# Kernel tuning notes

Measured on AMD Instinct MI355X. Metric: run time of the kernel, lower is better.

Reference implementation:

```python
import jax, jax.numpy as jnp
import numpy as np

B, T, F, D = 2, 1, 2112, 1024
H, DH = 8, 64
INNER = H * DH
NL = 721           # cls_dim(1) + num_latents(720)
VD = 64            # vis_dim // 4
DEPTH = 6
MAX_FRAMES = 2160
EPS = 1e-5
W_SCALE = 0.02


def _ln(x, g, b):
    m = jnp.mean(x, axis=-1, keepdims=True)
    v = jnp.mean(jnp.square(x - m), axis=-1, keepdims=True)
    return (x - m) * jax.lax.rsqrt(v + EPS) * g + b


def setup_inputs() -> dict:
    key = jax.random.key(0)
    ks = jax.random.split(key, 12)
    n = lambda k, shape, s=1.0: jax.random.normal(k, shape, dtype=jnp.float32) * s
    inp = {}
    inp['x'] = n(ks[0], (B, T, F, D))
    inp['split_sizes'] = jax.random.randint(ks[1], (B,), 0, F, dtype=jnp.int32)
    # resampler parameters (randn init like torch)
    inp['latents'] = n(ks[2], (NL, D))
    inp['spatial_embs'] = n(ks[3], (VD + 1, D))
    inp['frame_embs'] = n(ks[4], (MAX_FRAMES, D))
    # per-layer attention params (stacked over depth)
    inp['nm_g'] = jnp.ones((DEPTH, D)); inp['nm_b'] = jnp.zeros((DEPTH, D))
    inp['nl_g'] = jnp.ones((DEPTH, D)); inp['nl_b'] = jnp.zeros((DEPTH, D))
    inp['wq'] = n(ks[5], (DEPTH, D, INNER), W_SCALE)
    inp['wkv'] = n(ks[6], (DEPTH, D, 2 * INNER), W_SCALE)
    inp['wo'] = n(ks[7], (DEPTH, INNER, D), W_SCALE)
    # per-layer FFN params
    inp['ffn_g'] = jnp.ones((DEPTH, D)); inp['ffn_b'] = jnp.zeros((DEPTH, D))
    inp['ffw1'] = n(ks[8], (DEPTH, D, 4 * D), W_SCALE)
    inp['ffw2'] = n(ks[9], (DEPTH, 4 * D, D), W_SCALE)
    # final norm
    inp['final_g'] = jnp.ones((D,)); inp['final_b'] = jnp.zeros((D,))
    return inp


def reference(x, split_sizes, latents, spatial_embs, frame_embs,
              nm_g, nm_b, nl_g, nl_b, wq, wkv, wo,
              ffn_g, ffn_b, ffw1, ffw2, final_g, final_b):
    b, t, f, d = x.shape
    # spatial embeddings: first VD tokens get rows [:VD], rest get row [VD] broadcast
    add_sp = jnp.concatenate(
        [spatial_embs[:VD], jnp.broadcast_to(spatial_embs[VD:VD + 1], (f - VD, d))], axis=0)
    # frame embeddings: first VD tokens get row 0, frames get rows 1..f-VD
    add_fr = jnp.concatenate(
        [jnp.broadcast_to(frame_embs[0:1], (VD, d)), frame_embs[1:f - VD + 1]], axis=0)
    x = x + (add_sp + add_fr)  # broadcast over (b, t)

    lat = jnp.broadcast_to(latents, (b, t, NL, d))

    # variable-length mask over the x part of KV; latent positions never masked
    mask_x = jnp.arange(f)[None, :] >= split_sizes[:, None]              # (b, f)
    mask = jnp.concatenate([mask_x, jnp.zeros((b, NL), dtype=bool)], -1)  # (b, f+NL)
    mask = mask[:, None, None, None, :]                                   # (b,1,1,1,j)
    scale = DH ** -0.5

    for l in range(DEPTH):
        # --- PerceiverAttention ---
        xn = _ln(x, nm_g[l], nm_b[l])
        latn = _ln(lat, nl_g[l], nl_b[l])
        q = (latn @ wq[l]).reshape(b, t, NL, H, DH) * scale
        kv = jnp.concatenate([xn, latn], axis=-2) @ wkv[l]               # (b,t,f+NL,2*inner)
        k, v = jnp.split(kv, 2, axis=-1)
        k = k.reshape(b, t, f + NL, H, DH)
        v = v.reshape(b, t, f + NL, H, DH)
        sim = jnp.einsum('btihd,btjhd->bhtij', q, k)                     # (b,h,t,NL,f+NL)
        sim = sim - jax.lax.stop_gradient(jnp.max(sim, axis=-1, keepdims=True))
        sim = jnp.where(mask, -jnp.inf, sim)
        attn = jax.nn.softmax(sim, axis=-1)
        o = jnp.einsum('bhtij,btjhd->btihd', attn, v).reshape(b, t, NL, INNER)
        lat = lat + o @ wo[l]
        # --- FeedForward ---
        h1 = _ln(lat, ffn_g[l], ffn_b[l]) @ ffw1[l]
        lat = lat + jax.nn.gelu(h1, approximate=False) @ ffw2[l]

    return _ln(lat, final_g, final_b)
```

## Files before the change

kernel.cpp:

```cpp
#include <hip/hip_runtime.h>
#include <math.h>

constexpr int B = 2;
constexpr int F = 2112;
constexpr int D = 1024;
constexpr int H = 8;
constexpr int DH = 64;
constexpr int INNER = H * DH;
constexpr int NL = 721;
constexpr int NL_PAD = 768;
constexpr int MLAT = B * NL;
constexpr int MLAT_PAD = 1536;
constexpr int VD = 64;
constexpr int DEPTH = 6;
constexpr int FN = F + NL;
constexpr int FN_PAD = 2880;
constexpr int NBH = B * H;
constexpr int SKVMAX = 8;
constexpr int MX = B * F;
constexpr float EPS = 1e-5f;

typedef __bf16 bf16x8 __attribute__((ext_vector_type(8)));
typedef float  f32x4  __attribute__((ext_vector_type(4)));

static __device__ __forceinline__ unsigned short f2bf(float f)
{
    union { float f; unsigned int u; } x; x.f = f;
    unsigned int r = x.u + 0x7FFFu + ((x.u >> 16) & 1u);
    return (unsigned short)(r >> 16);
}
static __device__ __forceinline__ float bf2f(unsigned short u)
{
    union { unsigned int i; float f; } x; x.i = ((unsigned int)u) << 16; return x.f;
}

static __device__ __forceinline__ int xcd_swz(int b, int nt)
{
    return (b & 7) * (nt >> 3) + (b >> 3);
}

__device__ __forceinline__ void block_reduce_2(float& s, float& ss, float* red)
{
#pragma unroll
    for (int off = 32; off; off >>= 1) {
        s  += __shfl_xor(s, off);
        ss += __shfl_xor(ss, off);
    }
    int wv = threadIdx.x >> 6;
    if ((threadIdx.x & 63) == 0) { red[wv] = s; red[4 + wv] = ss; }
    __syncthreads();
    s  = red[0] + red[1] + red[2] + red[3];
    ss = red[4] + red[5] + red[6] + red[7];
}

__global__ __launch_bounds__(256) void emb_ln_kernel(
    const float* __restrict__ x, const float* __restrict__ sp_emb,
    const float* __restrict__ fr_emb, unsigned short* __restrict__ xhat)
{
    __shared__ float red[8];
    int r = blockIdx.x;
    int j = r % F;
    int t = threadIdx.x;
    const float4* xr = (const float4*)(x + (long)r * D);
    int spr = (j < VD) ? j : VD;
    int frr = (j < VD) ? 0 : (j - VD + 1);
    const float4* sp4 = (const float4*)(sp_emb + (long)spr * D);
    const float4* fr4 = (const float4*)(fr_emb + (long)frr * D);
    float4 v = xr[t], a = sp4[t], c = fr4[t];
    v.x += a.x + c.x; v.y += a.y + c.y; v.z += a.z + c.z; v.w += a.w + c.w;
    float s  = v.x + v.y + v.z + v.w;
    float ss = v.x*v.x + v.y*v.y + v.z*v.z + v.w*v.w;
    block_reduce_2(s, ss, red);
    float mean = s * (1.0f / D);
    float var  = ss * (1.0f / D) - mean * mean;
    float rstd = rsqrtf(var + EPS);
    ushort4 o;
    o.x = f2bf((v.x - mean) * rstd);
    o.y = f2bf((v.y - mean) * rstd);
    o.z = f2bf((v.z - mean) * rstd);
    o.w = f2bf((v.w - mean) * rstd);
    ((ushort4*)(xhat + (long)r * D))[t] = o;
}

__global__ __launch_bounds__(256) void prep_a_kernel(
    const unsigned short* __restrict__ xhat, const float* __restrict__ lat,
    const float* __restrict__ nmg, const float* __restrict__ nmb,
    const float* __restrict__ nlg, const float* __restrict__ nlb,
    unsigned short* __restrict__ xa, unsigned short* __restrict__ la)
{
    __shared__ float red[8];
    int r = blockIdx.x;
    int t = threadIdx.x;
    if (r < MX) {
        ushort4 u4 = ((const ushort4*)(xhat + (long)r * D))[t];
        float4 g4 = ((const float4*)nmg)[t];
        float4 b4 = ((const float4*)nmb)[t];
        ushort4 o;
        o.x = f2bf(bf2f(u4.x) * g4.x + b4.x);
        o.y = f2bf(bf2f(u4.y) * g4.y + b4.y);
        o.z = f2bf(bf2f(u4.z) * g4.z + b4.z);
        o.w = f2bf(bf2f(u4.w) * g4.w + b4.w);
        ((ushort4*)(xa + (long)r * D))[t] = o;
    } else {
        int rr = r - MX;
        float4 v = ((const float4*)(lat + (long)rr * D))[t];
        float s  = v.x + v.y + v.z + v.w;
        float ss = v.x*v.x + v.y*v.y + v.z*v.z + v.w*v.w;
        block_reduce_2(s, ss, red);
        float mean = s * (1.0f / D);
        float var  = ss * (1.0f / D) - mean * mean;
        float rstd = rsqrtf(var + EPS);
        float4 g4 = ((const float4*)nlg)[t];
        float4 b4 = ((const float4*)nlb)[t];
        ushort4 o;
        o.x = f2bf((v.x - mean) * rstd * g4.x + b4.x);
        o.y = f2bf((v.y - mean) * rstd * g4.y + b4.y);
        o.z = f2bf((v.z - mean) * rstd * g4.z + b4.z);
        o.w = f2bf((v.w - mean) * rstd * g4.w + b4.w);
        ((ushort4*)(la + (long)rr * D))[t] = o;
    }
}

__global__ __launch_bounds__(256) void rownorm_affine_bf16_kernel(
    const float* __restrict__ in, const float* __restrict__ g,
    const float* __restrict__ b, unsigned short* __restrict__ out)
{
    __shared__ float red[8];
    int r = blockIdx.x;
    int t = threadIdx.x;
    float4 v = ((const float4*)(in + (long)r * D))[t];
    float s  = v.x + v.y + v.z + v.w;
    float ss = v.x*v.x + v.y*v.y + v.z*v.z + v.w*v.w;
    block_reduce_2(s, ss, red);
    float mean = s * (1.0f / D);
    float var  = ss * (1.0f / D) - mean * mean;
    float rstd = rsqrtf(var + EPS);
    float4 g4 = ((const float4*)g)[t];
    float4 b4 = ((const float4*)b)[t];
    ushort4 o;
    o.x = f2bf((v.x - mean) * rstd * g4.x + b4.x);
    o.y = f2bf((v.y - mean) * rstd * g4.y + b4.y);
    o.z = f2bf((v.z - mean) * rstd * g4.z + b4.z);
    o.w = f2bf((v.w - mean) * rstd * g4.w + b4.w);
    ((ushort4*)(out + (long)r * D))[t] = o;
}

__global__ __launch_bounds__(256) void final_ln_kernel(
    const float* __restrict__ in, const float* __restrict__ g,
    const float* __restrict__ b, float* __restrict__ out)
{
    __shared__ float red[8];
    int r = blockIdx.x;
    int t = threadIdx.x;
    float4 v = ((const float4*)(in + (long)r * D))[t];
    float s  = v.x + v.y + v.z + v.w;
    float ss = v.x*v.x + v.y*v.y + v.z*v.z + v.w*v.w;
    block_reduce_2(s, ss, red);
    float mean = s * (1.0f / D);
    float var  = ss * (1.0f / D) - mean * mean;
    float rstd = rsqrtf(var + EPS);
    float4 g4 = ((const float4*)g)[t];
    float4 b4 = ((const float4*)b)[t];
    float4 o;
    o.x = (v.x - mean) * rstd * g4.x + b4.x;
    o.y = (v.y - mean) * rstd * g4.y + b4.y;
    o.z = (v.z - mean) * rstd * g4.z + b4.z;
    o.w = (v.w - mean) * rstd * g4.w + b4.w;
    ((float4*)(out + (long)r * D))[t] = o;
}

__global__ __launch_bounds__(256) void lat_init_kernel(
    const float* __restrict__ latents, float* __restrict__ lat)
{
    int r = blockIdx.x;
    int i = r % NL;
    int t = threadIdx.x;
    ((float4*)(lat + (long)r * D))[t] = ((const float4*)(latents + (long)i * D))[t];
}

constexpr long WL_LAT = 1536L * 1024;
constexpr long WL_WO  = 1024L * 512;
constexpr long WL_F1  = 4096L * 1024;
constexpr long WL_F2  = 1024L * 4096;
constexpr long WL_SZ  = WL_LAT + WL_WO + WL_F1 + WL_F2;

__device__ __forceinline__ void conv_tile64(
    const float* __restrict__ src, unsigned short* __restrict__ dst,
    int Kd, int Nd, int tn, int tk, float* lds)
{
    int t = threadIdx.x;
    int n0 = tn * 64, k0 = tk * 64;
#pragma unroll
    for (int p = 0; p < 16; ++p) {
        int idx = p * 256 + t;
        int kr = idx >> 6, nc = idx & 63;
        lds[nc * 65 + kr] = src[(long)(k0 + kr) * Nd + n0 + nc];
    }
    __syncthreads();
#pragma unroll
    for (int p = 0; p < 2; ++p) {
        int nl_ = p * 32 + (t >> 3);
        int kc  = t & 7;
        unsigned short u[8];
#pragma unroll
        for (int j = 0; j < 8; ++j)
            u[j] = f2bf(lds[nl_ * 65 + kc * 8 + j]);
        *(uint4*)(dst + (long)(n0 + nl_) * Kd + k0 + kc * 8) = *(uint4*)u;
    }
}

__global__ __launch_bounds__(256) void wt_conv_all_kernel(
    const float* __restrict__ wq, const float* __restrict__ wkv,
    const float* __restrict__ wo, const float* __restrict__ ffw1,
    const float* __restrict__ ffw2,
    unsigned short* __restrict__ wbuf, long wstride, int layer0)
{
    __shared__ float lds[64 * 65];
    int l = layer0 + blockIdx.y;
    unsigned short* wl = wbuf + (long)blockIdx.y * wstride;
    const float* wq_l   = wq   + (long)l * D * INNER;
    const float* wkv_l  = wkv  + (long)l * D * 2 * INNER;
    const float* wo_l   = wo   + (long)l * INNER * D;
    const float* ffw1_l = ffw1 + (long)l * D * 4 * D;
    const float* ffw2_l = ffw2 + (long)l * 4 * D * D;

    int T = blockIdx.x;
    if (T < 128) {
        conv_tile64(wq_l, wl, D, INNER, T & 7, T >> 3, lds);
    } else if (T < 384) {
        int Ti = T - 128;
        conv_tile64(wkv_l, wl + 512L * D, D, 2 * INNER, Ti & 15, Ti >> 4, lds);
    } else if (T < 512) {
        int Ti = T - 384;
        conv_tile64(wo_l, wl + WL_LAT, INNER, D, Ti & 15, Ti >> 4, lds);
    } else if (T < 1536) {
        int Ti = T - 512;
        conv_tile64(ffw1_l, wl + WL_LAT + WL_WO, D, 4 * D, Ti & 63, Ti >> 6, lds);
    } else {
        int Ti = T - 1536;
        conv_tile64(ffw2_l, wl + WL_LAT + WL_WO + WL_F1, 4 * D, D, Ti & 15, Ti >> 4, lds);
    }
}

__device__ __forceinline__ void load_set(
    const unsigned short* __restrict__ ap, const unsigned short* __restrict__ bp,
    long rs, int ko, bf16x8 (&av)[4], bf16x8 (&bv)[4])
{
#pragma unroll
    for (int q = 0; q < 4; ++q) {
        av[q] = *(const bf16x8*)(ap + q * rs + ko);
        bv[q] = *(const bf16x8*)(bp + q * rs + ko);
    }
}

__device__ __forceinline__ void mfma_set(
    const bf16x8 (&av)[4], const bf16x8 (&bv)[4], f32x4 (&acc)[4][4])
{
#pragma unroll
    for (int mm = 0; mm < 4; ++mm)
#pragma unroll
        for (int nn = 0; nn < 4; ++nn)
            acc[mm][nn] = __builtin_amdgcn_mfma_f32_16x16x32_bf16(av[mm], bv[nn], acc[mm][nn], 0, 0, 0);
}

__device__ __forceinline__ void gemm_core(
    const unsigned short* __restrict__ ap, const unsigned short* __restrict__ bp,
    long rs, int Kc, f32x4 (&acc)[4][4])
{
    bf16x8 aC[4], bC[4], aN[4], bN[4];
    load_set(ap, bp, rs, 0, aC, bC);
    for (int ko = 0; ko < Kc; ko += 64) {
        load_set(ap, bp, rs, ko + 32, aN, bN);
        mfma_set(aC, bC, acc);
        if (ko + 64 < Kc)
            load_set(ap, bp, rs, ko + 64, aC, bC);
        mfma_set(aN, bN, acc);
    }
}

__global__ __launch_bounds__(64) void qkv_fused_kernel(
    const unsigned short* __restrict__ la, const unsigned short* __restrict__ xa,
    const unsigned short* __restrict__ wlatT,
    unsigned short* __restrict__ qb, unsigned short* __restrict__ kb,
    unsigned short* __restrict__ vt)
{
    int lane = threadIdx.x;
    int lr = lane & 15, lg = lane >> 4;

    const unsigned short* A;
    const unsigned short* Bt;
    long m0, n0;
    int M, rpb, joff, qcols;
    int T = xcd_swz(blockIdx.x, 1608);
    if (T < 552) {
        int bm = T % 23, bn = T / 23;
        A = la; Bt = wlatT;
        m0 = (long)bm * 64; n0 = (long)bn * 64;
        M = MLAT; rpb = NL; joff = F; qcols = 512;
    } else {
        int Ti = T - 552;
        int bm = Ti % 66, bn = Ti / 66;
        A = xa; Bt = wlatT + 512L * D;
        m0 = (long)bm * 64; n0 = (long)bn * 64;
        M = MX; rpb = F; joff = 0; qcols = 0;
    }

    const unsigned short* ap = A  + (m0 + lr) * D + lg * 8;
    const unsigned short* bp = Bt + (n0 + lr) * D + lg * 8;
    f32x4 acc[4][4] = {};
    gemm_core(ap, bp, 16L * D, D, acc);

#pragma unroll
    for (int mm = 0; mm < 4; ++mm) {
        long ar0 = m0 + mm * 16 + lg * 4;
        if (ar0 >= M) continue;
#pragma unroll
        for (int nn = 0; nn < 4; ++nn) {
            long col = n0 + nn * 16 + lr;
            f32x4 v = acc[mm][nn];
            if (col < qcols) {
#pragma unroll
                for (int r = 0; r < 4; ++r) {
                    long ar = ar0 + r;
                    if (ar < M) {
                        int bb = ar >= NL;
                        long i = ar - (bb ? NL : 0);
                        qb[((long)bb * NL_PAD + i) * INNER + col] = f2bf(v[r] * 0.125f);
                    }
                }
            } else {
                int c = (int)col - qcols;
                if (c < 512) {
#pragma unroll
                    for (int r = 0; r < 4; ++r) {
                        long ar = ar0 + r;
                        if (ar < M) {
                            int bb = ar >= rpb;
                            long i = ar - (bb ? rpb : 0);
                            kb[((long)bb * FN_PAD + joff + i) * INNER + c] = f2bf(v[r]);
                        }
                    }
                } else {
                    int d = c - 512;
                    int bb0 = ar0 >= rpb;
                    int bb3 = (ar0 + 3) >= rpb;
                    long i0 = ar0 - (bb0 ? rpb : 0);
                    long j0 = joff + i0;
                    if ((ar0 + 3 < M) && (bb0 == bb3) && ((j0 & 3) == 0)) {
                        ushort4 pk;
                        pk.x = f2bf(v[0]); pk.y = f2bf(v[1]);
                        pk.z = f2bf(v[2]); pk.w = f2bf(v[3]);
                        *(ushort4*)(vt + ((long)bb0 * INNER + d) * FN_PAD + j0) = pk;
                    } else {
#pragma unroll
                        for (int r = 0; r < 4; ++r) {
                            long ar = ar0 + r;
                            if (ar < M) {
                                int bb = ar >= rpb;
                                long i = ar - (bb ? rpb : 0);
                                vt[((long)bb * INNER + d) * FN_PAD + joff + i] = f2bf(v[r]);
                            }
                        }
                    }
                }
            }
        }
    }
}

#define MODE_RESA  0
#define MODE_GELU  1

__global__ __launch_bounds__(64) void gemm_split_kernel(
    const unsigned short* __restrict__ A, const unsigned short* __restrict__ Bt,
    void* __restrict__ C, int M, int K, int Kc, int mode, int ldc,
    int bmN, int bnN)
{
    int lane = threadIdx.x;
    int lr = lane & 15, lg = lane >> 4;
    int u = xcd_swz(blockIdx.x, gridDim.x);
    int bm = u % bmN;
    int t2 = u / bmN;
    int bn = t2 % bnN;
    int kz = t2 / bnN;
    long m0 = (long)bm * 64;
    long n0 = (long)bn * 64;
    int k0 = kz * Kc;

    const unsigned short* ap = A  + (m0 + lr) * K + k0 + lg * 8;
    const unsigned short* bp = Bt + (n0 + lr) * K + k0 + lg * 8;
    f32x4 acc[4][4] = {};
    gemm_core(ap, bp, 16L * K, Kc, acc);

#pragma unroll
    for (int mm = 0; mm < 4; ++mm) {
        long ar0 = m0 + mm * 16 + lg * 4;
        if (ar0 >= M) continue;
#pragma unroll
        for (int nn = 0; nn < 4; ++nn) {
            long col = n0 + nn * 16 + lr;
            f32x4 v = acc[mm][nn];
            if (mode == MODE_RESA) {
                float* p = (float*)C;
#pragma unroll
                for (int r = 0; r < 4; ++r)
                    if (ar0 + r < M)
                        unsafeAtomicAdd(&p[(ar0 + r) * (long)ldc + col], v[r]);
            } else {
                unsigned short* p = (unsigned short*)C;
#pragma unroll
                for (int r = 0; r < 4; ++r)
                    if (ar0 + r < M) {
                        float val = v[r];
                        val = 0.5f * val * (1.0f + erff(val * 0.70710678118654752f));
                        p[(ar0 + r) * (long)ldc + col] = f2bf(val);
                    }
            }
        }
    }
}

__global__ __launch_bounds__(256) void attn_split_kernel(
    const unsigned short* __restrict__ qb, const unsigned short* __restrict__ kb,
    const unsigned short* __restrict__ vt, const int* __restrict__ split,
    float* __restrict__ po, float* __restrict__ pml, int skv)
{
    int u = xcd_swz(blockIdx.x, gridDim.x);
    int q64  = u % 12;
    int bh   = (u / 12) % NBH;
    int sidx = u / (12 * NBH);
    int b  = bh >> 3;
    int h  = bh & 7;
    int w  = threadIdx.x >> 6;
    int lane = threadIdx.x & 63;
    int q0 = q64 * 64 + w * 16;
    if (q0 >= NL) return;

    __shared__ unsigned short p_lds[4][16 * 64];
    unsigned short* pl = p_lds[w];

    int lr = lane & 15;
    int lg = lane >> 4;

    bf16x8 qa0, qa1;
    {
        const unsigned short* qrow = qb + ((long)b * NL_PAD + q0 + lr) * INNER + h * 64;
        qa0 = *(const bf16x8*)(qrow + lg * 8);
        qa1 = *(const bf16x8*)(qrow + 32 + lg * 8);
    }

    f32x4 oacc[4] = {{0,0,0,0},{0,0,0,0},{0,0,0,0},{0,0,0,0}};
    float m[4]    = {-1e30f, -1e30f, -1e30f, -1e30f};
    float lsum[4] = {0.f, 0.f, 0.f, 0.f};

    int sp = split[b];
    if (sp < 0) sp = 0;
    if (sp > F) sp = F;
    int ntx = (sp + 63) >> 6;
    int ntot = ntx + 12;
    int t0 = (ntot * sidx) / skv;
    int t1 = (ntot * (sidx + 1)) / skv;

    for (int t = t0; t < t1; ++t) {
        int j0, limit;
        if (t < ntx) { j0 = t * 64;             limit = sp; }
        else         { j0 = F + (t - ntx) * 64; limit = FN; }

        f32x4 s[4] = {{0,0,0,0},{0,0,0,0},{0,0,0,0},{0,0,0,0}};
        const unsigned short* kbase =
            kb + ((long)b * FN_PAD + j0 + lr) * INNER + h * 64 + lg * 8;
#pragma unroll
        for (int st = 0; st < 4; ++st) {
            bf16x8 kf0 = *(const bf16x8*)(kbase + (long)st * 16 * INNER);
            bf16x8 kf1 = *(const bf16x8*)(kbase + (long)st * 16 * INNER + 32);
            s[st] = __builtin_amdgcn_mfma_f32_16x16x32_bf16(qa0, kf0, s[st], 0, 0, 0);
            s[st] = __builtin_amdgcn_mfma_f32_16x16x32_bf16(qa1, kf1, s[st], 0, 0, 0);
        }

        if (j0 + 64 > limit) {
#pragma unroll
            for (int st = 0; st < 4; ++st) {
                bool valid = (j0 + st * 16 + lr) < limit;
#pragma unroll
                for (int r = 0; r < 4; ++r)
                    s[st][r] = valid ? s[st][r] : -1e30f;
            }
        }

        float tm[4];
#pragma unroll
        for (int r = 0; r < 4; ++r)
            tm[r] = fmaxf(fmaxf(s[0][r], s[1][r]), fmaxf(s[2][r], s[3][r]));
#pragma unroll
        for (int off = 1; off < 16; off <<= 1) {
#pragma unroll
            for (int r = 0; r < 4; ++r)
                tm[r] = fmaxf(tm[r], __shfl_xor(tm[r], off));
        }
        float cr[4];
#pragma unroll
        for (int r = 0; r < 4; ++r) {
            float mn = fmaxf(m[r], tm[r]);
            cr[r] = __expf(m[r] - mn);
            m[r]  = mn;
        }
#pragma unroll
        for (int st = 0; st < 4; ++st)
#pragma unroll
            for (int r = 0; r < 4; ++r)
                s[st][r] = __expf(s[st][r] - m[r]);
        float ts[4];
#pragma unroll
        for (int r = 0; r < 4; ++r)
            ts[r] = (s[0][r] + s[1][r]) + (s[2][r] + s[3][r]);
#pragma unroll
        for (int off = 1; off < 16; off <<= 1) {
#pragma unroll
            for (int r = 0; r < 4; ++r)
                ts[r] += __shfl_xor(ts[r], off);
        }
#pragma unroll
        for (int r = 0; r < 4; ++r)
            lsum[r] = lsum[r] * cr[r] + ts[r];
#pragma unroll
        for (int nst = 0; nst < 4; ++nst)
#pragma unroll
            for (int r = 0; r < 4; ++r)
                oacc[nst][r] *= cr[r];

#pragma unroll
        for (int st = 0; st < 4; ++st)
#pragma unroll
            for (int r = 0; r < 4; ++r) {
                int row  = lg * 4 + r;
                int col  = st * 16 + lr;
                int byte = (row * 128 + col * 2) ^ ((row & 7) << 4);
                *(unsigned short*)((char*)pl + byte) = f2bf(s[st][r]);
            }

#pragma unroll
        for (int kk = 0; kk < 2; ++kk) {
            int row  = lr;
            int byte = (row * 128 + kk * 64 + lg * 16) ^ ((row & 7) << 4);
            bf16x8 pa = *(const bf16x8*)((char*)pl + byte);
#pragma unroll
            for (int nst = 0; nst < 4; ++nst) {
                const unsigned short* vp =
                    vt + ((long)bh * DH + nst * 16 + lr) * FN_PAD + j0 + kk * 32 + lg * 8;
                bf16x8 vf = *(const bf16x8*)vp;
                oacc[nst] = __builtin_amdgcn_mfma_f32_16x16x32_bf16(pa, vf, oacc[nst], 0, 0, 0);
            }
        }
    }

    long base = ((long)sidx * NBH + bh) * NL_PAD;
#pragma unroll
    for (int nst = 0; nst < 4; ++nst)
#pragma unroll
        for (int r = 0; r < 4; ++r) {
            int row = q0 + lg * 4 + r;
            if (row < NL)
                po[(base + row) * DH + nst * 16 + lr] = oacc[nst][r];
        }
    if (lr == 0) {
#pragma unroll
        for (int r = 0; r < 4; ++r) {
            int row = q0 + lg * 4 + r;
            if (row < NL) {
                pml[(base + row) * 2 + 0] = m[r];
                pml[(base + row) * 2 + 1] = lsum[r];
            }
        }
    }
}

__global__ __launch_bounds__(256) void attn_combine_kernel(
    const float* __restrict__ po, const float* __restrict__ pml,
    unsigned short* __restrict__ o, int skv)
{
    int row = blockIdx.x * 4 + (threadIdx.x >> 6);
    if (row >= NBH * NL) return;
    int lane = threadIdx.x & 63;
    int bh = row / NL;
    int i  = row - bh * NL;
    int b = bh >> 3, h = bh & 7;

    float m = -1e30f, l = 0.0f, acc = 0.0f;
    for (int s = 0; s < skv; ++s) {
        long base = ((long)s * NBH + bh) * NL_PAD + i;
        float ms = pml[base * 2 + 0];
        float ls = pml[base * 2 + 1];
        float os = po[base * DH + lane];
        float mn = fmaxf(m, ms);
        float c1 = __expf(m - mn);
        float c2 = __expf(ms - mn);
        acc = acc * c1 + os * c2;
        l   = l * c1 + ls * c2;
        m   = mn;
    }
    o[((long)b * NL + i) * INNER + h * 64 + lane] = f2bf(acc / l);
}

extern "C" void kernel_launch(void* const* d_in, const int* in_sizes, int n_in,
                              void* d_out, int out_size, void* d_ws, size_t ws_size,
                              hipStream_t stream)
{
    const float* x        = (const float*)d_in[0];
    const int*   split    = (const int*)d_in[1];
    const float* latents  = (const float*)d_in[2];
    const float* sp_emb   = (const float*)d_in[3];
    const float* fr_emb   = (const float*)d_in[4];
    const float* nm_g     = (const float*)d_in[5];
    const float* nm_b     = (const float*)d_in[6];
    const float* nl_g     = (const float*)d_in[7];
    const float* nl_b     = (const float*)d_in[8];
    const float* wq       = (const float*)d_in[9];
    const float* wkv      = (const float*)d_in[10];
    const float* wo       = (const float*)d_in[11];
    const float* ffn_g    = (const float*)d_in[12];
    const float* ffn_b    = (const float*)d_in[13];
    const float* ffw1     = (const float*)d_in[14];
    const float* ffw2     = (const float*)d_in[15];
    const float* final_g  = (const float*)d_in[16];
    const float* final_b  = (const float*)d_in[17];
    float* out = (float*)d_out;

    char* cur = (char*)d_ws;
    auto alloc = [&](size_t bytes) {
        void* p = (void*)cur;
        cur += (bytes + 255) & ~(size_t)255;
        return p;
    };

    unsigned short* xhat = (unsigned short*)alloc((long)MX * D * 2);
    float* lat  = (float*)alloc((long)B * NL * D * 4);
    unsigned short* la  = (unsigned short*)alloc((long)MLAT_PAD * D * 2);
    unsigned short* fa  = (unsigned short*)alloc((long)MLAT_PAD * D * 2);
    unsigned short* h1b = (unsigned short*)alloc((long)MLAT_PAD * 4 * D * 2);
    unsigned short* ob  = (unsigned short*)alloc((long)MLAT_PAD * INNER * 2);
    unsigned short* qb  = (unsigned short*)alloc((long)B * NL_PAD * INNER * 2);
    unsigned short* kb  = (unsigned short*)alloc((long)B * FN_PAD * INNER * 2);
    unsigned short* vt  = (unsigned short*)alloc((long)B * FN_PAD * INNER * 2);
    unsigned short* xa  = (unsigned short*)alloc((long)MX * D * 2);
    float* pml = (float*)alloc((long)SKVMAX * NBH * NL_PAD * 2 * 4);

    size_t fixed = (size_t)(cur - (char*)d_ws);
    const size_t po8 = ((size_t)8 * NBH * NL_PAD * DH * 4 + 255) & ~(size_t)255;
    const size_t po4 = ((size_t)4 * NBH * NL_PAD * DH * 4 + 255) & ~(size_t)255;
    const size_t wb6 = ((size_t)6 * WL_SZ * 2 + 255) & ~(size_t)255;
    const size_t wb1 = ((size_t)WL_SZ * 2 + 255) & ~(size_t)255;
    const size_t margin = 4096;

    int skv;
    bool hoist_w;
    if (fixed + po8 + wb6 + margin <= ws_size)      { skv = 8; hoist_w = true;  }
    else if (fixed + po4 + wb6 + margin <= ws_size) { skv = 4; hoist_w = true;  }
    else if (fixed + po8 + wb1 + margin <= ws_size) { skv = 8; hoist_w = false; }
    else                                            { skv = 4; hoist_w = false; }

    float* po = (float*)alloc(skv == 8 ? po8 : po4);
    unsigned short* wbuf = (unsigned short*)alloc(hoist_w ? wb6 : wb1);

    emb_ln_kernel<<<MX, 256, 0, stream>>>(x, sp_emb, fr_emb, xhat);
    lat_init_kernel<<<B * NL, 256, 0, stream>>>(latents, lat);

    if (hoist_w)
        wt_conv_all_kernel<<<dim3(2560, 6), 256, 0, stream>>>(
            wq, wkv, wo, ffw1, ffw2, wbuf, WL_SZ, 0);

    for (int l = 0; l < DEPTH; ++l) {
        unsigned short* wl = wbuf + (hoist_w ? (long)l * WL_SZ : 0);
        if (!hoist_w)
            wt_conv_all_kernel<<<dim3(2560, 1), 256, 0, stream>>>(
                wq, wkv, wo, ffw1, ffw2, wbuf, 0, l);

        unsigned short* wlatT = wl;
        unsigned short* woT   = wl + WL_LAT;
        unsigned short* f1T   = wl + WL_LAT + WL_WO;
        unsigned short* f2T   = wl + WL_LAT + WL_WO + WL_F1;

        prep_a_kernel<<<MX + MLAT, 256, 0, stream>>>(
            xhat, lat, nm_g + (long)l * D, nm_b + (long)l * D,
            nl_g + (long)l * D, nl_b + (long)l * D, xa, la);

        qkv_fused_kernel<<<1608, 64, 0, stream>>>(la, xa, wlatT, qb, kb, vt);

        attn_split_kernel<<<12 * NBH * skv, 256, 0, stream>>>(
            qb, kb, vt, split, po, pml, skv);
        attn_combine_kernel<<<(NBH * NL + 3) / 4, 256, 0, stream>>>(po, pml, ob, skv);

        gemm_split_kernel<<<23 * 16 * 4, 64, 0, stream>>>(
            ob, woT, lat, MLAT, INNER, 128, MODE_RESA, D, 23, 16);

        rownorm_affine_bf16_kernel<<<MLAT, 256, 0, stream>>>(
            lat, ffn_g + (long)l * D, ffn_b + (long)l * D, fa);
        gemm_split_kernel<<<23 * 64, 64, 0, stream>>>(
            fa, f1T, h1b, MLAT, D, D, MODE_GELU, 4 * D, 23, 64);
        gemm_split_kernel<<<23 * 16 * 8, 64, 0, stream>>>(
            h1b, f2T, lat, MLAT, 4 * D, 512, MODE_RESA, D, 23, 16);
    }

    final_ln_kernel<<<MLAT, 256, 0, stream>>>(lat, final_g, final_b, out);
}
```

Baseline: 1.890 ms.

## Fold LayerNorm gamma/beta into weights and precomputed biases, drop per-layer x affine pass

LayerNorm scale vectors are folded into the bf16 weight conversion, and the shift vectors are turned into per-layer output biases (beta @ W) computed once by a new bias kernel. The K/V projection of x now reads the shared normalized xhat directly, with a separate gamma-scaled weight block, so the per-layer pass that rewrote the full 4224x1024 x activation is removed. The weight conversion tile is widened to 128 rows along K. The cost is extra weight storage for the x-side KV block, a naive serial-K bias kernel, and slightly different bf16 rounding because gamma is applied before quantization.

```diff
diff --git a/kernel.cpp b/kernel.cpp
--- a/kernel.cpp
+++ b/kernel.cpp
@@ -18,6 +18,7 @@
 constexpr int NBH = B * H;
 constexpr int SKVMAX = 8;
 constexpr int MX = B * F;
+constexpr int NBIAS = 6656;
 constexpr float EPS = 1e-5f;
 
 typedef __bf16 bf16x8 __attribute__((ext_vector_type(8)));
@@ -82,48 +83,8 @@
     ((ushort4*)(xhat + (long)r * D))[t] = o;
 }
 
-__global__ __launch_bounds__(256) void prep_a_kernel(
-    const unsigned short* __restrict__ xhat, const float* __restrict__ lat,
-    const float* __restrict__ nmg, const float* __restrict__ nmb,
-    const float* __restrict__ nlg, const float* __restrict__ nlb,
-    unsigned short* __restrict__ xa, unsigned short* __restrict__ la)
-{
-    __shared__ float red[8];
-    int r = blockIdx.x;
-    int t = threadIdx.x;
-    if (r < MX) {
-        ushort4 u4 = ((const ushort4*)(xhat + (long)r * D))[t];
-        float4 g4 = ((const float4*)nmg)[t];
-        float4 b4 = ((const float4*)nmb)[t];
-        ushort4 o;
-        o.x = f2bf(bf2f(u4.x) * g4.x + b4.x);
-        o.y = f2bf(bf2f(u4.y) * g4.y + b4.y);
-        o.z = f2bf(bf2f(u4.z) * g4.z + b4.z);
-        o.w = f2bf(bf2f(u4.w) * g4.w + b4.w);
-        ((ushort4*)(xa + (long)r * D))[t] = o;
-    } else {
-        int rr = r - MX;
-        float4 v = ((const float4*)(lat + (long)rr * D))[t];
-        float s  = v.x + v.y + v.z + v.w;
-        float ss = v.x*v.x + v.y*v.y + v.z*v.z + v.w*v.w;
-        block_reduce_2(s, ss, red);
-        float mean = s * (1.0f / D);
-        float var  = ss * (1.0f / D) - mean * mean;
-        float rstd = rsqrtf(var + EPS);
-        float4 g4 = ((const float4*)nlg)[t];
-        float4 b4 = ((const float4*)nlb)[t];
-        ushort4 o;
-        o.x = f2bf((v.x - mean) * rstd * g4.x + b4.x);
-        o.y = f2bf((v.y - mean) * rstd * g4.y + b4.y);
-        o.z = f2bf((v.z - mean) * rstd * g4.z + b4.z);
-        o.w = f2bf((v.w - mean) * rstd * g4.w + b4.w);
-        ((ushort4*)(la + (long)rr * D))[t] = o;
-    }
-}
-
-__global__ __launch_bounds__(256) void rownorm_affine_bf16_kernel(
-    const float* __restrict__ in, const float* __restrict__ g,
-    const float* __restrict__ b, unsigned short* __restrict__ out)
+__global__ __launch_bounds__(256) void rownorm_plain_kernel(
+    const float* __restrict__ in, unsigned short* __restrict__ out)
 {
     __shared__ float red[8];
     int r = blockIdx.x;
@@ -135,13 +96,11 @@
     float mean = s * (1.0f / D);
     float var  = ss * (1.0f / D) - mean * mean;
     float rstd = rsqrtf(var + EPS);
-    float4 g4 = ((const float4*)g)[t];
-    float4 b4 = ((const float4*)b)[t];
     ushort4 o;
-    o.x = f2bf((v.x - mean) * rstd * g4.x + b4.x);
-    o.y = f2bf((v.y - mean) * rstd * g4.y + b4.y);
-    o.z = f2bf((v.z - mean) * rstd * g4.z + b4.z);
-    o.w = f2bf((v.w - mean) * rstd * g4.w + b4.w);
+    o.x = f2bf((v.x - mean) * rstd);
+    o.y = f2bf((v.y - mean) * rstd);
+    o.z = f2bf((v.z - mean) * rstd);
+    o.w = f2bf((v.w - mean) * rstd);
     ((ushort4*)(out + (long)r * D))[t] = o;
 }
 
@@ -178,34 +137,56 @@
     ((float4*)(lat + (long)r * D))[t] = ((const float4*)(latents + (long)i * D))[t];
 }
 
+__global__ __launch_bounds__(256) void bias_kernel(
+    const float* __restrict__ wq, const float* __restrict__ wkv,
+    const float* __restrict__ ffw1,
+    const float* __restrict__ nl_b, const float* __restrict__ nm_b,
+    const float* __restrict__ ffn_b, float* __restrict__ bias)
+{
+    int l = blockIdx.y;
+    int o = blockIdx.x * 256 + threadIdx.x;
+    const float* W; const float* bv; int n, Nd;
+    if (o < 512)       { W = wq   + (long)l * D * INNER;    bv = nl_b  + (long)l * D; n = o;        Nd = INNER; }
+    else if (o < 1536) { W = wkv  + (long)l * D * 2 * INNER; bv = nl_b + (long)l * D; n = o - 512;  Nd = 2 * INNER; }
+    else if (o < 2560) { W = wkv  + (long)l * D * 2 * INNER; bv = nm_b + (long)l * D; n = o - 1536; Nd = 2 * INNER; }
+    else               { W = ffw1 + (long)l * D * 4 * D;     bv = ffn_b + (long)l * D; n = o - 2560; Nd = 4 * D; }
+    float s = 0.f;
+    for (int k = 0; k < D; ++k)
+        s += bv[k] * W[(long)k * Nd + n];
+    bias[(long)l * NBIAS + o] = s;
+}
+
 constexpr long WL_LAT = 1536L * 1024;
+constexpr long WL_KVX = 1024L * 1024;
 constexpr long WL_WO  = 1024L * 512;
 constexpr long WL_F1  = 4096L * 1024;
 constexpr long WL_F2  = 1024L * 4096;
-constexpr long WL_SZ  = WL_LAT + WL_WO + WL_F1 + WL_F2;
-
-__device__ __forceinline__ void conv_tile64(
+constexpr long WL_SZ  = WL_LAT + WL_KVX + WL_WO + WL_F1 + WL_F2;
+
+__device__ __forceinline__ void conv_tile128(
     const float* __restrict__ src, unsigned short* __restrict__ dst,
-    int Kd, int Nd, int tn, int tk, float* lds)
+    int Kd, int Nd, int tn, int tk, const float* __restrict__ g, float* lds)
 {
     int t = threadIdx.x;
-    int n0 = tn * 64, k0 = tk * 64;
-#pragma unroll
-    for (int p = 0; p < 16; ++p) {
+    int n0 = tn * 64, k0 = tk * 128;
+#pragma unroll
+    for (int p = 0; p < 32; ++p) {
         int idx = p * 256 + t;
         int kr = idx >> 6, nc = idx & 63;
-        lds[nc * 65 + kr] = src[(long)(k0 + kr) * Nd + n0 + nc];
+        float val = src[(long)(k0 + kr) * Nd + n0 + nc];
+        if (g) val *= g[k0 + kr];
+        lds[nc * 129 + kr] = val;
     }
     __syncthreads();
 #pragma unroll
-    for (int p = 0; p < 2; ++p) {
-        int nl_ = p * 32 + (t >> 3);
-        int kc  = t & 7;
+    for (int p = 0; p < 4; ++p) {
+        int nr = p * 16 + (t >> 4);
+        int kc = t & 15;
         unsigned short u[8];
 #pragma unroll
         for (int j = 0; j < 8; ++j)
-            u[j] = f2bf(lds[nl_ * 65 + kc * 8 + j]);
-        *(uint4*)(dst + (long)(n0 + nl_) * Kd + k0 + kc * 8) = *(uint4*)u;
+            u[j] = f2bf(lds[nr * 129 + kc * 8 + j]);
+        *(uint4*)(dst + (long)(n0 + nr) * Kd + k0 + kc * 8) = *(uint4*)u;
     }
 }
 
@@ -213,9 +194,11 @@
     const float* __restrict__ wq, const float* __restrict__ wkv,
     const float* __restrict__ wo, const float* __restrict__ ffw1,
     const float* __restrict__ ffw2,
+    const float* __restrict__ nl_g, const float* __restrict__ nm_g,
+    const float* __restrict__ ffn_g,
     unsigned short* __restrict__ wbuf, long wstride, int layer0)
 {
-    __shared__ float lds[64 * 65];
+    __shared__ float lds[64 * 129];
     int l = layer0 + blockIdx.y;
     unsigned short* wl = wbuf + (long)blockIdx.y * wstride;
     const float* wq_l   = wq   + (long)l * D * INNER;
@@ -223,22 +206,28 @@
     const float* wo_l   = wo   + (long)l * INNER * D;
     const float* ffw1_l = ffw1 + (long)l * D * 4 * D;
     const float* ffw2_l = ffw2 + (long)l * 4 * D * D;
+    const float* nlg = nl_g + (long)l * D;
+    const float* nmg = nm_g + (long)l * D;
+    const float* ffg = ffn_g + (long)l * D;
 
     int T = blockIdx.x;
-    if (T < 128) {
-        conv_tile64(wq_l, wl, D, INNER, T & 7, T >> 3, lds);
+    if (T < 64) {
+        conv_tile128(wq_l, wl, D, INNER, T & 7, T >> 3, nlg, lds);
+    } else if (T < 192) {
+        int Ti = T - 64;
+        conv_tile128(wkv_l, wl + 512L * D, D, 2 * INNER, Ti & 15, Ti >> 4, nlg, lds);
+    } else if (T < 320) {
+        int Ti = T - 192;
+        conv_tile128(wkv_l, wl + WL_LAT, D, 2 * INNER, Ti & 15, Ti >> 4, nmg, lds);
     } else if (T < 384) {
-        int Ti = T - 128;
-        conv_tile64(wkv_l, wl + 512L * D, D, 2 * INNER, Ti & 15, Ti >> 4, lds);
-    } else if (T < 512) {
+        int Ti = T - 320;
+        conv_tile128(wo_l, wl + WL_LAT + WL_KVX, INNER, D, Ti & 15, Ti >> 4, nullptr, lds);
+    } else if (T < 896) {
         int Ti = T - 384;
-        conv_tile64(wo_l, wl + WL_LAT, INNER, D, Ti & 15, Ti >> 4, lds);
-    } else if (T < 1536) {
-        int Ti = T - 512;
-        conv_tile64(ffw1_l, wl + WL_LAT + WL_WO, D, 4 * D, Ti & 63, Ti >> 6, lds);
+        conv_tile128(ffw1_l, wl + WL_LAT + WL_KVX + WL_WO, D, 4 * D, Ti & 63, Ti >> 6, ffg, lds);
     } else {
-        int Ti = T - 1536;
-        conv_tile64(ffw2_l, wl + WL_LAT + WL_WO + WL_F1, 4 * D, D, Ti & 15, Ti >> 4, lds);
+        int Ti = T - 896;
+        conv_tile128(ffw2_l, wl + WL_LAT + WL_KVX + WL_WO + WL_F1, 4 * D, D, Ti & 15, Ti >> 4, nullptr, lds);
     }
 }
 
@@ -279,8 +268,8 @@
 }
 
 __global__ __launch_bounds__(64) void qkv_fused_kernel(
-    const unsigned short* __restrict__ la, const unsigned short* __restrict__ xa,
-    const unsigned short* __restrict__ wlatT,
+    const unsigned short* __restrict__ la, const unsigned short* __restrict__ xhat,
+    const unsigned short* __restrict__ wlatT, const float* __restrict__ bias_l,
     unsigned short* __restrict__ qb, unsigned short* __restrict__ kb,
     unsigned short* __restrict__ vt)
 {
@@ -291,18 +280,19 @@
     const unsigned short* Bt;
     long m0, n0;
     int M, rpb, joff, qcols;
+    bool isLat;
     int T = xcd_swz(blockIdx.x, 1608);
     if (T < 552) {
         int bm = T % 23, bn = T / 23;
         A = la; Bt = wlatT;
         m0 = (long)bm * 64; n0 = (long)bn * 64;
-        M = MLAT; rpb = NL; joff = F; qcols = 512;
+        M = MLAT; rpb = NL; joff = F; qcols = 512; isLat = true;
     } else {
         int Ti = T - 552;
         int bm = Ti % 66, bn = Ti / 66;
-        A = xa; Bt = wlatT + 512L * D;
+        A = xhat; Bt = wlatT + WL_LAT;
         m0 = (long)bm * 64; n0 = (long)bn * 64;
-        M = MX; rpb = F; joff = 0; qcols = 0;
+        M = MX; rpb = F; joff = 0; qcols = 0; isLat = false;
     }
 
     const unsigned short* ap = A  + (m0 + lr) * D + lg * 8;
@@ -317,7 +307,10 @@
 #pragma unroll
         for (int nn = 0; nn < 4; ++nn) {
             long col = n0 + nn * 16 + lr;
+            float bcol = isLat ? bias_l[col] : bias_l[1536 + col];
             f32x4 v = acc[mm][nn];
+#pragma unroll
+            for (int r = 0; r < 4; ++r) v[r] += bcol;
             if (col < qcols) {
 #pragma unroll
                 for (int r = 0; r < 4; ++r) {
@@ -373,8 +366,8 @@
 
 __global__ __launch_bounds__(64) void gemm_split_kernel(
     const unsigned short* __restrict__ A, const unsigned short* __restrict__ Bt,
-    void* __restrict__ C, int M, int K, int Kc, int mode, int ldc,
-    int bmN, int bnN)
+    void* __restrict__ C, const float* __restrict__ bias,
+    int M, int K, int Kc, int mode, int ldc, int bmN, int bnN)
 {
     int lane = threadIdx.x;
     int lr = lane & 15, lg = lane >> 4;
@@ -407,11 +400,12 @@
                     if (ar0 + r < M)
                         unsafeAtomicAdd(&p[(ar0 + r) * (long)ldc + col], v[r]);
             } else {
+                float bcol = bias ? bias[col] : 0.f;
                 unsigned short* p = (unsigned short*)C;
 #pragma unroll
                 for (int r = 0; r < 4; ++r)
                     if (ar0 + r < M) {
-                        float val = v[r];
+                        float val = v[r] + bcol;
                         val = 0.5f * val * (1.0f + erff(val * 0.70710678118654752f));
                         p[(ar0 + r) * (long)ldc + col] = f2bf(val);
                     }
@@ -641,8 +635,8 @@
     unsigned short* qb  = (unsigned short*)alloc((long)B * NL_PAD * INNER * 2);
     unsigned short* kb  = (unsigned short*)alloc((long)B * FN_PAD * INNER * 2);
     unsigned short* vt  = (unsigned short*)alloc((long)B * FN_PAD * INNER * 2);
-    unsigned short* xa  = (unsigned short*)alloc((long)MX * D * 2);
-    float* pml = (float*)alloc((long)SKVMAX * NBH * NL_PAD * 2 * 4);
+    float* bias = (float*)alloc((long)DEPTH * NBIAS * 4);
+    float* pml  = (float*)alloc((long)SKVMAX * NBH * NL_PAD * 2 * 4);
 
     size_t fixed = (size_t)(cur - (char*)d_ws);
     const size_t po8 = ((size_t)8 * NBH * NL_PAD * DH * 4 + 255) & ~(size_t)255;
@@ -663,41 +657,41 @@
 
     emb_ln_kernel<<<MX, 256, 0, stream>>>(x, sp_emb, fr_emb, xhat);
     lat_init_kernel<<<B * NL, 256, 0, stream>>>(latents, lat);
+    bias_kernel<<<dim3(NBIAS / 256, 6), 256, 0, stream>>>(
+        wq, wkv, ffw1, nl_b, nm_b, ffn_b, bias);
 
     if (hoist_w)
-        wt_conv_all_kernel<<<dim3(2560, 6), 256, 0, stream>>>(
-            wq, wkv, wo, ffw1, ffw2, wbuf, WL_SZ, 0);
+        wt_conv_all_kernel<<<dim3(1408, 6), 256, 0, stream>>>(
+            wq, wkv, wo, ffw1, ffw2, nl_g, nm_g, ffn_g, wbuf, WL_SZ, 0);
 
     for (int l = 0; l < DEPTH; ++l) {
         unsigned short* wl = wbuf + (hoist_w ? (long)l * WL_SZ : 0);
         if (!hoist_w)
-            wt_conv_all_kernel<<<dim3(2560, 1), 256, 0, stream>>>(
-                wq, wkv, wo, ffw1, ffw2, wbuf, 0, l);
+            wt_conv_all_kernel<<<dim3(1408, 1), 256, 0, stream>>>(
+                wq, wkv, wo, ffw1, ffw2, nl_g, nm_g, ffn_g, wbuf, 0, l);
 
         unsigned short* wlatT = wl;
-        unsigned short* woT   = wl + WL_LAT;
-        unsigned short* f1T   = wl + WL_LAT + WL_WO;
-        unsigned short* f2T   = wl + WL_LAT + WL_WO + WL_F1;
-
-        prep_a_kernel<<<MX + MLAT, 256, 0, stream>>>(
-            xhat, lat, nm_g + (long)l * D, nm_b + (long)l * D,
-            nl_g + (long)l * D, nl_b + (long)l * D, xa, la);
-
-        qkv_fused_kernel<<<1608, 64, 0, stream>>>(la, xa, wlatT, qb, kb, vt);
+        unsigned short* woT   = wl + WL_LAT + WL_KVX;
+        unsigned short* f1T   = wl + WL_LAT + WL_KVX + WL_WO;
+        unsigned short* f2T   = wl + WL_LAT + WL_KVX + WL_WO + WL_F1;
+        const float* bias_l = bias + (long)l * NBIAS;
+
+        rownorm_plain_kernel<<<MLAT, 256, 0, stream>>>(lat, la);
+
+        qkv_fused_kernel<<<1608, 64, 0, stream>>>(la, xhat, wlatT, bias_l, qb, kb, vt);
 
         attn_split_kernel<<<12 * NBH * skv, 256, 0, stream>>>(
             qb, kb, vt, split, po, pml, skv);
         attn_combine_kernel<<<(NBH * NL + 3) / 4, 256, 0, stream>>>(po, pml, ob, skv);
 
         gemm_split_kernel<<<23 * 16 * 4, 64, 0, stream>>>(
-            ob, woT, lat, MLAT, INNER, 128, MODE_RESA, D, 23, 16);
-
-        rownorm_affine_bf16_kernel<<<MLAT, 256, 0, stream>>>(
-            lat, ffn_g + (long)l * D, ffn_b + (long)l * D, fa);
+            ob, woT, lat, nullptr, MLAT, INNER, 128, MODE_RESA, D, 23, 16);
+
+        rownorm_plain_kernel<<<MLAT, 256, 0, stream>>>(lat, fa);
         gemm_split_kernel<<<23 * 64, 64, 0, stream>>>(
-            fa, f1T, h1b, MLAT, D, D, MODE_GELU, 4 * D, 23, 64);
+            fa, f1T, h1b, bias_l + 2560, MLAT, D, D, MODE_GELU, 4 * D, 23, 64);
         gemm_split_kernel<<<23 * 16 * 8, 64, 0, stream>>>(
-            h1b, f2T, lat, MLAT, 4 * D, 512, MODE_RESA, D, 23, 16);
+            h1b, f2T, lat, nullptr, MLAT, 4 * D, 512, MODE_RESA, D, 23, 16);
     }
 
     final_ln_kernel<<<MLAT, 256, 0, stream>>>(lat, final_g, final_b, out);
```

Measured after the change: 1.991 ms. +5.3%, slower.
